# Kernel optimization log

Measured on AMD Instinct MI355X. Metric: run time of the kernel, lower is better.

The kernel has to match this reference:

```python
import jax, jax.numpy as jnp
import numpy as np

PAD = 32      # person_attrs_dim
NZ = 64       # num_zones
T = 32768     # number of timesteps
D = PAD + 1 + NZ  # 97, input dim to the MLP


def _ln(x, g, b, eps=1e-5):
    # LayerNorm over the last (only) axis of a 1-D vector
    m = jnp.mean(x)
    v = jnp.mean((x - m) ** 2)
    return g * (x - m) / jnp.sqrt(v + eps) + b


def setup_inputs() -> dict:
    key = jax.random.key(0)
    ks = jax.random.split(key, 24)

    def xav(k, shape):  # xavier_normal_ for nn.Linear weight [out, in]
        std = np.sqrt(2.0 / (shape[0] + shape[1])).astype(np.float32)
        return std * jax.random.normal(k, shape, dtype=jnp.float32)

    def lng(k, n):  # layernorm gain (perturbed from 1 so grads are non-trivial)
        return 1.0 + 0.1 * jax.random.normal(k, (n,), dtype=jnp.float32)

    def lnb(k, n):
        return 0.1 * jax.random.normal(k, (n,), dtype=jnp.float32)

    inp = {
        "person_attrs": jax.random.normal(ks[0], (PAD,), dtype=jnp.float32),
        "times": jax.random.uniform(ks[1], (T,), dtype=jnp.float32) * 24.0,
        "zone_features": jax.random.normal(ks[2], (NZ, 16), dtype=jnp.float32),
        "edge_index": jax.random.randint(ks[3], (2, 256), 0, NZ, dtype=jnp.int32),
        # input_norm
        "g0": lng(ks[4], D), "b0": lnb(ks[5], D),
        # encoder1: Linear(D,256) + LN(256)
        "W1": xav(ks[6], (256, D)), "b1": jnp.zeros((256,), jnp.float32),
        "g1": lng(ks[7], 256), "be1": lnb(ks[8], 256),
        # encoder2: Linear(256,128) + LN(128)
        "W2": xav(ks[9], (128, 256)), "b2": jnp.zeros((128,), jnp.float32),
        "g2": lng(ks[10], 128), "be2": lnb(ks[11], 128),
        # output_layer: Linear(128,64) + LN(64) + Linear(64,NZ)
        "W3": xav(ks[12], (64, 128)), "b3": jnp.zeros((64,), jnp.float32),
        "g3": lng(ks[13], 64), "be3": lnb(ks[14], 64),
        "W4": xav(ks[15], (NZ, 64)), "b4": jnp.zeros((NZ,), jnp.float32),
    }
    return inp


def reference(person_attrs, times, zone_features, edge_index,
              g0, b0, W1, b1, g1, be1, W2, b2, g2, be2,
              W3, b3, g3, be3, W4, b4):
    nz = W4.shape[0]
    # set_graph_data: symmetric adjacency with self-loops (zone_features unused)
    u, v = edge_index[0], edge_index[1]
    A = jnp.zeros((nz, nz), jnp.float32).at[u, v].set(1.0).at[v, u].set(1.0)
    A = jnp.maximum(A, jnp.eye(nz, dtype=jnp.float32))

    def step(zone, t):
        onehot = jax.nn.one_hot(zone, nz, dtype=jnp.float32)
        x = jnp.concatenate([person_attrs, t[None], onehot])  # [D]
        x = _ln(x, g0, b0)
        h = jax.nn.relu(_ln(W1 @ x + b1, g1, be1))   # dropout is eval-mode identity
        h = jax.nn.relu(_ln(W2 @ h + b2, g2, be2))
        h = jax.nn.relu(_ln(W3 @ h + b3, g3, be3))
        raw = W4 @ h + b4                            # [nz] raw logits
        row = A[zone]
        # (raw/temp with invalid=-50/temp) * temp  ==  where(valid, raw, -50)
        pred = jnp.where(row > 0, raw, jnp.float32(-50.0))
        nxt = jnp.argmax(jnp.where(row > 0, raw, -jnp.inf)).astype(zone.dtype)
        return nxt, pred

    _, zone_logits = jax.lax.scan(step, jnp.array(0, jnp.int32), times)
    return zone_logits  # [T, nz]
```

## Files before the change

kernel.cpp:

```cpp
#include <hip/hip_runtime.h>
#include <stdint.h>

typedef __attribute__((ext_vector_type(8))) short bf16x8;
typedef __attribute__((ext_vector_type(4))) float f32x4;
typedef __attribute__((ext_vector_type(4))) unsigned int u32x4;
typedef __attribute__((ext_vector_type(2))) unsigned int u32x2;

#define MFMA(a, b, c) __builtin_amdgcn_mfma_f32_16x16x32_bf16(a, b, c, 0, 0, 0)

__device__ __forceinline__ unsigned short f2b(float x) {
  unsigned u = __float_as_uint(x);
  return (unsigned short)((u + 0x7fffu + ((u >> 16) & 1u)) >> 16);
}
__device__ __forceinline__ float b2f(unsigned short h) {
  return __uint_as_float(((unsigned)h) << 16);
}

struct u2 { unsigned hi, lo; };
__device__ __forceinline__ u2 split2(float h0, float h1) {
  unsigned u0 = __float_as_uint(h0), u1 = __float_as_uint(h1);
  u2 r;
  r.hi = (u0 >> 16) | (u1 & 0xffff0000u);
  float r0 = h0 - __uint_as_float(u0 & 0xffff0000u);
  float r1 = h1 - __uint_as_float(u1 & 0xffff0000u);
  r.lo = (__float_as_uint(r0) >> 16) | (__float_as_uint(r1) & 0xffff0000u);
  return r;
}

#define SWZ(row, col) ((col) ^ ((((row) >> 2) & 1) << 4) ^ ((((row) >> 3) & 1) << 2))


__global__ void k_prep(const float* __restrict__ pa, const float* __restrict__ g0,
                       const float* __restrict__ b0, const float* __restrict__ W1,
                       const float* __restrict__ b1,
                       float* __restrict__ c_pa, float* __restrict__ w_t,
                       float* __restrict__ c_g, float* __restrict__ c_const,
                       float* __restrict__ scal, float* __restrict__ wzT,
                       float* __restrict__ wzZ) {
  int j = threadIdx.x;
  const float* wr = W1 + j * 97;
  float cg = 0.f, cc = 0.f, cp = 0.f;
  for (int k = 0; k < 97; ++k) { float w = wr[k]; cg += w * g0[k]; cc += w * b0[k]; }
  for (int k = 0; k < 32; ++k) cp += wr[k] * g0[k] * pa[k];
  c_g[j] = cg;
  c_const[j] = cc + b1[j];
  c_pa[j] = cp;
  w_t[j] = wr[32] * g0[32];
  for (int z = 0; z < 64; ++z) {
    float v = wr[33 + z] * g0[33 + z];
    wzT[j * 64 + z] = v;
    wzZ[z * 256 + j] = v;
  }
  if (j == 0) {
    float s = 0.f, q = 0.f;
    for (int k = 0; k < 32; ++k) { float x = pa[k]; s += x; q += x * x; }
    scal[0] = s; scal[1] = q;
  }
}

__global__ void k_prep2(const float* __restrict__ c_pa, const float* __restrict__ w_t,
                        const float* __restrict__ c_g, const float* __restrict__ c_const,
                        const float* __restrict__ wzT, float* __restrict__ st) {
  int tid = threadIdx.x;
  if (tid < 64) {
    int z = tid;
    float A = 0.f, Q = 0.f, dpa = 0.f, dwt = 0.f, dcg = 0.f, dcc = 0.f;
    for (int k = 0; k < 256; ++k) {
      float wz = wzT[k * 64 + z];
      A += wz; Q = fmaf(wz, wz, Q);
      dpa = fmaf(c_pa[k], wz, dpa);
      dwt = fmaf(w_t[k], wz, dwt);
      dcg = fmaf(c_g[k], wz, dcg);
      dcc = fmaf(c_const[k], wz, dcc);
    }
    st[z] = A; st[64 + z] = Q; st[128 + z] = dpa;
    st[192 + z] = dwt; st[256 + z] = dcg; st[320 + z] = dcc;
  } else {
    int lane = tid - 64;
    float acc[14];
    #pragma unroll
    for (int m = 0; m < 14; ++m) acc[m] = 0.f;
    for (int k = lane; k < 256; k += 64) {
      float P = c_pa[k], W = w_t[k], G = c_g[k], C = c_const[k];
      acc[0] += P; acc[1] += W; acc[2] += G; acc[3] += C;
      acc[4] = fmaf(P, P, acc[4]); acc[5] = fmaf(P, W, acc[5]);
      acc[6] = fmaf(P, G, acc[6]); acc[7] = fmaf(P, C, acc[7]);
      acc[8] = fmaf(W, W, acc[8]); acc[9] = fmaf(W, G, acc[9]);
      acc[10] = fmaf(W, C, acc[10]); acc[11] = fmaf(G, G, acc[11]);
      acc[12] = fmaf(G, C, acc[12]); acc[13] = fmaf(C, C, acc[13]);
    }
    #pragma unroll
    for (int off = 1; off < 64; off <<= 1) {
      #pragma unroll
      for (int m = 0; m < 14; ++m) acc[m] += __shfl_xor(acc[m], off, 64);
    }
    if (lane == 0) {
      #pragma unroll
      for (int m = 0; m < 14; ++m) st[386 + m] = acc[m];
    }
  }
}

__global__ void k_scal2st(const float* __restrict__ scal, float* __restrict__ st) {
  if (threadIdx.x < 2) st[384 + threadIdx.x] = scal[threadIdx.x];
}

__global__ void k_adj(const int* __restrict__ ei, unsigned long long* __restrict__ adj) {
  int t = threadIdx.x;
  if (t < 64) adj[t] = 1ull << t;
  __syncthreads();
  int u = ei[t] & 63, v = ei[256 + t] & 63;
  atomicOr(&adj[u], 1ull << v);
  atomicOr(&adj[v], 1ull << u);
}

__global__ void k_wsplit(const float* __restrict__ W2, const float* __restrict__ W3,
                         const float* __restrict__ W4,
                         unsigned short* __restrict__ W2Ah, unsigned short* __restrict__ W2Al,
                         unsigned short* __restrict__ W3Ah, unsigned short* __restrict__ W3Al,
                         unsigned short* __restrict__ W4Ah, unsigned short* __restrict__ W4Al) {
  int idx = blockIdx.x * 256 + threadIdx.x;
  float w; unsigned short* ph; unsigned short* pl; int o;
  if (idx < 32768) {
    int mt = idx >> 12, kt = (idx >> 9) & 7, lane = (idx >> 3) & 63, j = idx & 7;
    int m = mt * 16 + (lane & 15), k = kt * 32 + (lane >> 4) * 8 + j;
    w = W2[m * 256 + k]; ph = W2Ah; pl = W2Al; o = idx;
  } else if (idx < 40960) {
    int r = idx - 32768;
    int mt = r >> 11, kt = (r >> 9) & 3, lane = (r >> 3) & 63, j = r & 7;
    int m = mt * 16 + (lane & 15), k = kt * 32 + (lane >> 4) * 8 + j;
    w = W3[m * 128 + k]; ph = W3Ah; pl = W3Al; o = r;
  } else if (idx < 45056) {
    int r = idx - 40960;
    int mt = r >> 10, kt = (r >> 9) & 1, lane = (r >> 3) & 63, j = r & 7;
    int m = mt * 16 + (lane & 15), k = kt * 32 + (lane >> 4) * 8 + j;
    w = W4[m * 64 + k]; ph = W4Ah; pl = W4Al; o = r;
  } else return;
  unsigned short hb = f2b(w);
  ph[o] = hb;
  pl[o] = f2b(w - b2f(hb));
}


__global__ __launch_bounds__(256, 5) void k_pass1(
    const float* __restrict__ times,
    const float* __restrict__ c_pa, const float* __restrict__ w_t,
    const float* __restrict__ c_g, const float* __restrict__ c_const,
    const float* __restrict__ wzT, const float* __restrict__ st,
    const unsigned short* __restrict__ W2Ah, const unsigned short* __restrict__ W2Al,
    const unsigned short* __restrict__ W3Ah, const unsigned short* __restrict__ W3Al,
    const unsigned short* __restrict__ W4Ah, const unsigned short* __restrict__ W4Al,
    const float* __restrict__ b2, const float* __restrict__ b3,
    const float* __restrict__ b4,
    const float* __restrict__ g1, const float* __restrict__ be1,
    const float* __restrict__ g2, const float* __restrict__ be2,
    const float* __restrict__ g3, const float* __restrict__ be3,
    const unsigned long long* __restrict__ adj,
    unsigned char* __restrict__ nxt) {
  __shared__ __align__(16) char region[16384];
  __shared__ float u_lds[256];
  __shared__ float ps[512];

  unsigned short* Bhi = (unsigned short*)region;
  unsigned short* Blo = (unsigned short*)(region + 8192);
  unsigned long long* pk = (unsigned long long*)ps;

  const int tid = threadIdx.x;
  const int lane = tid & 63;
  const int l15 = lane & 15;
  const int lhi = lane >> 4;
  const int w = __builtin_amdgcn_readfirstlane(tid >> 6);
  const int i = blockIdx.x;

  const float t = times[i];
  const float m0 = (st[384] + t + 1.0f) * (1.0f / 97.0f);
  const float e2 = (st[385] + t * t + 1.0f) * (1.0f / 97.0f);
  const float alpha = 1.0f / sqrtf(e2 - m0 * m0 + 1e-5f);
  const float gma = -m0 * alpha;

  const f32x4 zero4 = {0.f, 0.f, 0.f, 0.f};

  {
    int k = tid;
    float u = fmaf(t, w_t[k], c_pa[k]);
    u = fmaf(alpha, u, c_const[k]);
    u = fmaf(gma, c_g[k], u);
    u_lds[k] = u;
    float su = u, sq = u * u;
    #pragma unroll
    for (int off = 1; off < 64; off <<= 1) {
      su += __shfl_xor(su, off, 64);
      sq += __shfl_xor(sq, off, 64);
    }
    if (lane == 0) { ps[w] = su; ps[256 + w] = sq; }
  }
  __syncthreads();
  float mu1, inv1;
  {
    float U1 = ps[0] + ps[1] + ps[2] + ps[3];
    float Qu = ps[256] + ps[257] + ps[258] + ps[259];
    float A1 = st[lane], Qz = st[64 + lane];
    float dpa = st[128 + lane], dwt = st[192 + lane];
    float dcg = st[256 + lane], dcc = st[320 + lane];
    float s1 = fmaf(alpha, A1, U1);
    float uwz = fmaf(alpha, fmaf(t, dwt, dpa), fmaf(gma, dcg, dcc));
    float s2 = Qu + 2.0f * alpha * uwz + alpha * alpha * Qz;
    mu1 = s1 * (1.0f / 256.0f);
    inv1 = 1.0f / sqrtf(s2 * (1.0f / 256.0f) - mu1 * mu1 + 1e-5f);
  }

  f32x4 acc[2][4];
  #pragma unroll
  for (int a = 0; a < 2; ++a)
    #pragma unroll
    for (int b = 0; b < 4; ++b) acc[a][b] = zero4;

  for (int kc = 0; kc < 4; ++kc) {
    if (kc) __syncthreads();
    #pragma unroll
    for (int q = 0; q < 2; ++q) {
      int o = w * 2 + q;
      int kb = kc * 64 + o * 8;
      f32x4 u0 = *(const f32x4*)(u_lds + kb);
      f32x4 u1v = *(const f32x4*)(u_lds + kb + 4);
      float hbuf[8];
      #pragma unroll
      for (int j = 0; j < 8; ++j) {
        int k = kb + j;
        float u = (j < 4) ? u0[j] : u1v[j - 4];
        float p = fmaf(alpha, wzT[k * 64 + lane], u);
        float gi = g1[k] * inv1;
        float bb = fmaf(-mu1, gi, be1[k]);
        hbuf[j] = fmaxf(fmaf(p, gi, bb), 0.f);
      }
      u32x4 vh, vl;
      #pragma unroll
      for (int e = 0; e < 4; ++e) {
        u2 s = split2(hbuf[2 * e], hbuf[2 * e + 1]);
        vh[e] = s.hi; vl[e] = s.lo;
      }
      int slotd = (((o >> 2) * 4 + lhi) * 64 + (o & 3) * 16 + l15) * 4;
      *(u32x4*)((unsigned*)Bhi + slotd) = vh;
      *(u32x4*)((unsigned*)Blo + slotd) = vl;
    }
    __syncthreads();
    #pragma unroll
    for (int kt = 0; kt < 2; ++kt) {
      int ktg = kc * 2 + kt;
      bf16x8 a0h = *(const bf16x8*)(W2Ah + (((2 * w + 0) * 8 + ktg) * 64 + lane) * 8);
      bf16x8 a0l = *(const bf16x8*)(W2Al + (((2 * w + 0) * 8 + ktg) * 64 + lane) * 8);
      bf16x8 a1h = *(const bf16x8*)(W2Ah + (((2 * w + 1) * 8 + ktg) * 64 + lane) * 8);
      bf16x8 a1l = *(const bf16x8*)(W2Al + (((2 * w + 1) * 8 + ktg) * 64 + lane) * 8);
      #pragma unroll
      for (int nt = 0; nt < 4; ++nt) {
        bf16x8 bh = *(const bf16x8*)(Bhi + ((kt * 4 + nt) * 64 + lane) * 8);
        bf16x8 bl = *(const bf16x8*)(Blo + ((kt * 4 + nt) * 64 + lane) * 8);
        acc[0][nt] = MFMA(a0h, bh, acc[0][nt]);
        acc[0][nt] = MFMA(a0h, bl, acc[0][nt]);
        acc[0][nt] = MFMA(a0l, bh, acc[0][nt]);
        acc[1][nt] = MFMA(a1h, bh, acc[1][nt]);
        acc[1][nt] = MFMA(a1h, bl, acc[1][nt]);
        acc[1][nt] = MFMA(a1l, bh, acc[1][nt]);
      }
    }
  }

  #pragma unroll
  for (int mti = 0; mti < 2; ++mti) {
    f32x4 bv = *(const f32x4*)(b2 + w * 32 + mti * 16 + lhi * 4);
    #pragma unroll
    for (int nt = 0; nt < 4; ++nt) acc[mti][nt] += bv;
  }
  #pragma unroll
  for (int nt = 0; nt < 4; ++nt) {
    float x1 = 0.f, x2 = 0.f;
    #pragma unroll
    for (int mti = 0; mti < 2; ++mti)
      #pragma unroll
      for (int r = 0; r < 4; ++r) { float v = acc[mti][nt][r]; x1 += v; x2 += v * v; }
    x1 += __shfl_xor(x1, 16, 64); x1 += __shfl_xor(x1, 32, 64);
    x2 += __shfl_xor(x2, 16, 64); x2 += __shfl_xor(x2, 32, 64);
    if (lane < 16) {
      ps[w * 64 + nt * 16 + lane] = x1;
      ps[256 + w * 64 + nt * 16 + lane] = x2;
    }
  }
  __syncthreads();
  if (w == 0) {
    int c = lane;
    float a = ps[c] + ps[64 + c] + ps[128 + c] + ps[192 + c];
    float b = ps[256 + c] + ps[320 + c] + ps[384 + c] + ps[448 + c];
    float mu = a * (1.0f / 128.0f);
    float inv = 1.0f / sqrtf(b * (1.0f / 128.0f) - mu * mu + 1e-5f);
    ps[c] = inv;
    ps[64 + c] = -mu * inv;
  }
  __syncthreads();

  f32x4 acc2[4];
  #pragma unroll
  for (int b = 0; b < 4; ++b) acc2[b] = zero4;

  for (int kc2 = 0; kc2 < 2; ++kc2) {
    if ((w >> 1) == kc2) {
      f32x4 g2v[2], be2v[2];
      #pragma unroll
      for (int mti = 0; mti < 2; ++mti) {
        g2v[mti]  = *(const f32x4*)(g2  + w * 32 + mti * 16 + lhi * 4);
        be2v[mti] = *(const f32x4*)(be2 + w * 32 + mti * 16 + lhi * 4);
      }
      #pragma unroll
      for (int nt = 0; nt < 4; ++nt) {
        int c = nt * 16 + l15;
        float P = ps[c], Q = ps[64 + c];
        #pragma unroll
        for (int mti = 0; mti < 2; ++mti) {
          float h[4];
          #pragma unroll
          for (int r = 0; r < 4; ++r) {
            float G = g2v[mti][r];
            h[r] = fmaxf(fmaf(acc[mti][nt][r], G * P, fmaf(G, Q, be2v[mti][r])), 0.f);
          }
          u2 s01 = split2(h[0], h[1]);
          u2 s23 = split2(h[2], h[3]);
          int base = (((w - 2 * kc2) * 4 + nt) * 64 +
                      (mti * 2 + (lhi >> 1)) * 16 + l15) * 8 + (lhi & 1) * 4;
          u32x2 vh = {s01.hi, s23.hi};
          u32x2 vl = {s01.lo, s23.lo};
          *(u32x2*)(Bhi + base) = vh;
          *(u32x2*)(Blo + base) = vl;
        }
      }
    }
    __syncthreads();
    #pragma unroll
    for (int kt = 0; kt < 2; ++kt) {
      int ktg = kc2 * 2 + kt;
      bf16x8 ah = *(const bf16x8*)(W3Ah + ((w * 4 + ktg) * 64 + lane) * 8);
      bf16x8 al = *(const bf16x8*)(W3Al + ((w * 4 + ktg) * 64 + lane) * 8);
      #pragma unroll
      for (int nt = 0; nt < 4; ++nt) {
        bf16x8 bh = *(const bf16x8*)(Bhi + ((kt * 4 + nt) * 64 + lane) * 8);
        bf16x8 bl = *(const bf16x8*)(Blo + ((kt * 4 + nt) * 64 + lane) * 8);
        acc2[nt] = MFMA(ah, bh, acc2[nt]);
        acc2[nt] = MFMA(ah, bl, acc2[nt]);
        acc2[nt] = MFMA(al, bh, acc2[nt]);
      }
    }
    __syncthreads();
  }

  {
    f32x4 bv = *(const f32x4*)(b3 + w * 16 + lhi * 4);
    #pragma unroll
    for (int nt = 0; nt < 4; ++nt) acc2[nt] += bv;
  }
  #pragma unroll
  for (int nt = 0; nt < 4; ++nt) {
    float x1 = 0.f, x2 = 0.f;
    #pragma unroll
    for (int r = 0; r < 4; ++r) { float v = acc2[nt][r]; x1 += v; x2 += v * v; }
    x1 += __shfl_xor(x1, 16, 64); x1 += __shfl_xor(x1, 32, 64);
    x2 += __shfl_xor(x2, 16, 64); x2 += __shfl_xor(x2, 32, 64);
    if (lane < 16) {
      ps[w * 64 + nt * 16 + lane] = x1;
      ps[256 + w * 64 + nt * 16 + lane] = x2;
    }
  }
  __syncthreads();
  if (w == 0) {
    int c = lane;
    float a = ps[c] + ps[64 + c] + ps[128 + c] + ps[192 + c];
    float b = ps[256 + c] + ps[320 + c] + ps[384 + c] + ps[448 + c];
    float mu = a * (1.0f / 64.0f);
    float inv = 1.0f / sqrtf(b * (1.0f / 64.0f) - mu * mu + 1e-5f);
    ps[c] = inv;
    ps[64 + c] = -mu * inv;
  }
  __syncthreads();

  {
    f32x4 g3v  = *(const f32x4*)(g3  + w * 16 + lhi * 4);
    f32x4 be3v = *(const f32x4*)(be3 + w * 16 + lhi * 4);
    #pragma unroll
    for (int nt = 0; nt < 4; ++nt) {
      int c = nt * 16 + l15;
      float P = ps[c], Q = ps[64 + c];
      float h[4];
      #pragma unroll
      for (int r = 0; r < 4; ++r) {
        float G = g3v[r];
        h[r] = fmaxf(fmaf(acc2[nt][r], G * P, fmaf(G, Q, be3v[r])), 0.f);
      }
      u2 s01 = split2(h[0], h[1]);
      u2 s23 = split2(h[2], h[3]);
      int base = (((w >> 1) * 4 + nt) * 64 +
                  ((w & 1) * 2 + (lhi >> 1)) * 16 + l15) * 8 + (lhi & 1) * 4;
      u32x2 vh = {s01.hi, s23.hi};
      u32x2 vl = {s01.lo, s23.lo};
      *(u32x2*)(Bhi + base) = vh;
      *(u32x2*)(Blo + base) = vl;
    }
  }
  __syncthreads();

  f32x4 acc3[4];
  #pragma unroll
  for (int b = 0; b < 4; ++b) acc3[b] = zero4;
  #pragma unroll
  for (int kt = 0; kt < 2; ++kt) {
    bf16x8 ah = *(const bf16x8*)(W4Ah + ((w * 2 + kt) * 64 + lane) * 8);
    bf16x8 al = *(const bf16x8*)(W4Al + ((w * 2 + kt) * 64 + lane) * 8);
    #pragma unroll
    for (int nt = 0; nt < 4; ++nt) {
      bf16x8 bh = *(const bf16x8*)(Bhi + ((kt * 4 + nt) * 64 + lane) * 8);
      bf16x8 bl = *(const bf16x8*)(Blo + ((kt * 4 + nt) * 64 + lane) * 8);
      acc3[nt] = MFMA(ah, bh, acc3[nt]);
      acc3[nt] = MFMA(ah, bl, acc3[nt]);
      acc3[nt] = MFMA(al, bh, acc3[nt]);
    }
  }
  f32x4 b4v = *(const f32x4*)(b4 + w * 16 + lhi * 4);
  unsigned long long kbest[4];
  #pragma unroll
  for (int nt = 0; nt < 4; ++nt) {
    unsigned long long am = adj[nt * 16 + l15];
    unsigned long long kb = 0ull;
    #pragma unroll
    for (int r = 0; r < 4; ++r) {
      int o = w * 16 + lhi * 4 + r;
      float raw = acc3[nt][r] + b4v[r];
      float val = ((am >> o) & 1ull) ? raw : -__builtin_huge_valf();
      unsigned u = __float_as_uint(val);
      u = (u & 0x80000000u) ? ~u : (u | 0x80000000u);
      unsigned long long key = ((unsigned long long)u << 6) | (unsigned long long)(63 - o);
      if (key > kb) kb = key;
    }
    unsigned long long oth = __shfl_xor(kb, 16, 64); if (oth > kb) kb = oth;
    oth = __shfl_xor(kb, 32, 64); if (oth > kb) kb = oth;
    kbest[nt] = kb;
  }
  if (lane < 16) {
    #pragma unroll
    for (int nt = 0; nt < 4; ++nt) pk[w * 64 + nt * 16 + lane] = kbest[nt];
  }
  __syncthreads();
  if (tid < 64) {
    unsigned long long k0 = pk[tid], k1 = pk[64 + tid];
    unsigned long long k2 = pk[128 + tid], k3 = pk[192 + tid];
    unsigned long long a = k0 > k1 ? k0 : k1;
    unsigned long long b = k2 > k3 ? k2 : k3;
    unsigned long long bb = a > b ? a : b;
    nxt[(size_t)i * 64 + tid] = (unsigned char)(63u - (unsigned)(bb & 63ull));
  }
}


__global__ void k_scan_a(const unsigned char* __restrict__ nxt,
                         unsigned char* __restrict__ cmap) {
  int c = blockIdx.x, lane = threadIdx.x;
  int g = lane;
  const unsigned char* p = nxt + (size_t)c * 128 * 64;
  for (int s = 0; s < 128; ++s) {
    int sig = p[s * 64 + lane];
    g = __shfl(sig, g, 64);
  }
  cmap[c * 64 + lane] = (unsigned char)g;
}

__global__ void k_scan_b(const unsigned char* __restrict__ cmap,
                         int* __restrict__ startz) {
  int lane = threadIdx.x;
  int cur = 0;
  for (int c = 0; c < 256; ++c) {
    if (lane == 0) startz[c] = cur;
    int row = cmap[c * 64 + lane];
    cur = __shfl(row, cur, 64);
  }
}

__global__ void k_scan_c(const unsigned char* __restrict__ nxt,
                         const int* __restrict__ startz,
                         unsigned char* __restrict__ zones) {
  int c = blockIdx.x, lane = threadIdx.x;
  int cur = startz[c];
  const unsigned char* p = nxt + (size_t)c * 128 * 64;
  for (int s = 0; s < 128; ++s) {
    if (lane == 0) zones[c * 128 + s] = (unsigned char)cur;
    int row = p[s * 64 + lane];
    cur = __shfl(row, cur, 64);
  }
}


__global__ __launch_bounds__(256, 2) void k_pass2m(
    const float* __restrict__ times, const unsigned char* __restrict__ zones,
    const float* __restrict__ c_pa, const float* __restrict__ w_t,
    const float* __restrict__ c_g, const float* __restrict__ c_const,
    const float* __restrict__ wzZ, const float* __restrict__ st,
    const unsigned short* __restrict__ W2Ah, const unsigned short* __restrict__ W2Al,
    const unsigned short* __restrict__ W3Ah, const unsigned short* __restrict__ W3Al,
    const unsigned short* __restrict__ W4Ah, const unsigned short* __restrict__ W4Al,
    const float* __restrict__ b2, const float* __restrict__ b3,
    const float* __restrict__ b4,
    const float* __restrict__ g1, const float* __restrict__ be1,
    const float* __restrict__ g2, const float* __restrict__ be2,
    const float* __restrict__ g3, const float* __restrict__ be3,
    const unsigned long long* __restrict__ adj,
    float* __restrict__ out) {
  __shared__ __align__(16) char region[32768];
  __shared__ float ps1[256], ps2[256];
  __shared__ unsigned long long am_lds[64];

  unsigned short* B1hi = (unsigned short*)region;
  unsigned short* B1lo = (unsigned short*)(region + 16384);
  float* h2p = (float*)region;
  unsigned short* B2hi = (unsigned short*)region;
  unsigned short* B2lo = (unsigned short*)(region + 16384);
  float* h3p = (float*)region;
  unsigned short* B3hi = (unsigned short*)(region + 16384);
  unsigned short* B3lo = (unsigned short*)(region + 24576);
  float* outT = (float*)region;

  const int tid = threadIdx.x;
  const int lane = tid & 63;
  const int l15 = lane & 15;
  const int lhi = lane >> 4;
  const int w = __builtin_amdgcn_readfirstlane(tid >> 6);
  const int i0 = blockIdx.x * 64;

  const float t = times[i0 + lane];
  const int z = zones[i0 + lane];
  const int zrow = z << 8;
  if (tid < 64) am_lds[tid] = adj[zones[i0 + tid]];

  const float m0 = (st[384] + t + 1.0f) * (1.0f / 97.0f);
  const float e2 = (st[385] + t * t + 1.0f) * (1.0f / 97.0f);
  const float a0 = 1.0f / sqrtf(e2 - m0 * m0 + 1e-5f);
  const float a1 = a0 * t;
  const float a2 = -m0 * a0;

  float mu1, inv1;
  {
    float SP = st[386], SW = st[387], SG = st[388], SC = st[389];
    float PP = st[390], PW = st[391], PG = st[392], PC = st[393];
    float WW = st[394], WG = st[395], WC = st[396];
    float GG = st[397], GC = st[398], CC = st[399];
    float U1 = a0 * SP + a1 * SW + a2 * SG + SC;
    float s1 = fmaf(a0, st[z], U1);
    float Qu = a0 * a0 * PP + a1 * a1 * WW + a2 * a2 * GG + CC
             + 2.0f * (a0 * a1 * PW + a0 * a2 * PG + a0 * PC
                       + a1 * a2 * WG + a1 * WC + a2 * GC);
    float uwz = a0 * st[128 + z] + a1 * st[192 + z] + a2 * st[256 + z] + st[320 + z];
    float s2 = Qu + 2.0f * a0 * uwz + a0 * a0 * st[64 + z];
    mu1 = s1 * (1.0f / 256.0f);
    inv1 = 1.0f / sqrtf(s2 * (1.0f / 256.0f) - mu1 * mu1 + 1e-5f);
  }

  const f32x4 zero4 = {0.f, 0.f, 0.f, 0.f};
  f32x4 acc[2][4];
  #pragma unroll
  for (int a = 0; a < 2; ++a)
    #pragma unroll
    for (int b = 0; b < 4; ++b) acc[a][b] = zero4;

  for (int kc = 0; kc < 2; ++kc) {
    if (kc) __syncthreads();
    #pragma unroll
    for (int q = 0; q < 4; ++q) {
      int kb = kc * 128 + w * 32 + q * 8;
      float hbuf[8];
      #pragma unroll
      for (int j = 0; j < 8; ++j) {
        int k = kb + j;
        float u = fmaf(a0, c_pa[k], fmaf(a1, w_t[k], fmaf(a2, c_g[k], c_const[k])));
        float p = fmaf(a0, wzZ[zrow + k], u);
        float gi = g1[k] * inv1;
        float bb = fmaf(-mu1, gi, be1[k]);
        hbuf[j] = fmaxf(fmaf(p, gi, bb), 0.f);
      }
      u32x4 vh, vl;
      #pragma unroll
      for (int e = 0; e < 4; ++e) {
        u2 s = split2(hbuf[2 * e], hbuf[2 * e + 1]);
        vh[e] = s.hi; vl[e] = s.lo;
      }
      int slotd = ((w * 4 + lhi) * 64 + q * 16 + l15) * 4;
      *(u32x4*)((unsigned*)B1hi + slotd) = vh;
      *(u32x4*)((unsigned*)B1lo + slotd) = vl;
    }
    __syncthreads();
    for (int kt = 0; kt < 4; ++kt) {
      int ktg = kc * 4 + kt;
      bf16x8 a0h = *(const bf16x8*)(W2Ah + (((2 * w + 0) * 8 + ktg) * 64 + lane) * 8);
      bf16x8 a0l = *(const bf16x8*)(W2Al + (((2 * w + 0) * 8 + ktg) * 64 + lane) * 8);
      bf16x8 a1h = *(const bf16x8*)(W2Ah + (((2 * w + 1) * 8 + ktg) * 64 + lane) * 8);
      bf16x8 a1l = *(const bf16x8*)(W2Al + (((2 * w + 1) * 8 + ktg) * 64 + lane) * 8);
      #pragma unroll
      for (int nt = 0; nt < 4; ++nt) {
        bf16x8 bh = *(const bf16x8*)(B1hi + ((kt * 4 + nt) * 64 + lane) * 8);
        bf16x8 bl = *(const bf16x8*)(B1lo + ((kt * 4 + nt) * 64 + lane) * 8);
        acc[0][nt] = MFMA(a0h, bh, acc[0][nt]);
        acc[0][nt] = MFMA(a0h, bl, acc[0][nt]);
        acc[0][nt] = MFMA(a0l, bh, acc[0][nt]);
        acc[1][nt] = MFMA(a1h, bh, acc[1][nt]);
        acc[1][nt] = MFMA(a1h, bl, acc[1][nt]);
        acc[1][nt] = MFMA(a1l, bh, acc[1][nt]);
      }
    }
  }
  #pragma unroll
  for (int mti = 0; mti < 2; ++mti) {
    f32x4 bv = *(const f32x4*)(b2 + w * 32 + mti * 16 + lhi * 4);
    #pragma unroll
    for (int nt = 0; nt < 4; ++nt) acc[mti][nt] += bv;
  }
  {
    float sa[4], sb[4];
    #pragma unroll
    for (int nt = 0; nt < 4; ++nt) {
      float x1 = 0.f, x2 = 0.f;
      #pragma unroll
      for (int mti = 0; mti < 2; ++mti)
        #pragma unroll
        for (int r = 0; r < 4; ++r) { float v = acc[mti][nt][r]; x1 += v; x2 += v * v; }
      x1 += __shfl_xor(x1, 16, 64); x1 += __shfl_xor(x1, 32, 64);
      x2 += __shfl_xor(x2, 16, 64); x2 += __shfl_xor(x2, 32, 64);
      sa[nt] = x1; sb[nt] = x2;
    }
    if (lane < 16) {
      #pragma unroll
      for (int nt = 0; nt < 4; ++nt) {
        ps1[w * 64 + nt * 16 + lane] = sa[nt];
        ps2[w * 64 + nt * 16 + lane] = sb[nt];
      }
    }
  }
  __syncthreads();
  #pragma unroll
  for (int mti = 0; mti < 2; ++mti)
    #pragma unroll
    for (int nt = 0; nt < 4; ++nt)
      #pragma unroll
      for (int r = 0; r < 4; ++r) {
        int row = w * 32 + mti * 16 + lhi * 4 + r;
        h2p[row * 64 + SWZ(row, nt * 16 + l15)] = acc[mti][nt][r];
      }
  __syncthreads();

  float mu2, inv2;
  {
    float a = ps1[lane] + ps1[64 + lane] + ps1[128 + lane] + ps1[192 + lane];
    float b = ps2[lane] + ps2[64 + lane] + ps2[128 + lane] + ps2[192 + lane];
    mu2 = a * (1.0f / 128.0f);
    inv2 = 1.0f / sqrtf(b * (1.0f / 128.0f) - mu2 * mu2 + 1e-5f);
  }
  float hv[32];
  #pragma unroll
  for (int mi = 0; mi < 32; ++mi) {
    int row = w * 32 + mi;
    hv[mi] = h2p[row * 64 + SWZ(row, lane)];
  }
  __syncthreads();
  #pragma unroll
  for (int q = 0; q < 4; ++q) {
    float hbuf[8];
    #pragma unroll
    for (int j = 0; j < 8; ++j) {
      int mi = q * 8 + j, mm = w * 32 + mi;
      float gi = g2[mm] * inv2;
      float bb = fmaf(-mu2, gi, be2[mm]);
      hbuf[j] = fmaxf(fmaf(hv[mi], gi, bb), 0.f);
    }
    u32x4 vh, vl;
    #pragma unroll
    for (int e = 0; e < 4; ++e) {
      u2 s = split2(hbuf[2 * e], hbuf[2 * e + 1]);
      vh[e] = s.hi; vl[e] = s.lo;
    }
    int slotd = ((w * 4 + lhi) * 64 + q * 16 + l15) * 4;
    *(u32x4*)((unsigned*)B2hi + slotd) = vh;
    *(u32x4*)((unsigned*)B2lo + slotd) = vl;
  }
  __syncthreads();

  f32x4 acc2[4];
  #pragma unroll
  for (int b = 0; b < 4; ++b) acc2[b] = zero4;
  for (int kt = 0; kt < 4; ++kt) {
    bf16x8 ah = *(const bf16x8*)(W3Ah + ((w * 4 + kt) * 64 + lane) * 8);
    bf16x8 al = *(const bf16x8*)(W3Al + ((w * 4 + kt) * 64 + lane) * 8);
    #pragma unroll
    for (int nt = 0; nt < 4; ++nt) {
      bf16x8 bh = *(const bf16x8*)(B2hi + ((kt * 4 + nt) * 64 + lane) * 8);
      bf16x8 bl = *(const bf16x8*)(B2lo + ((kt * 4 + nt) * 64 + lane) * 8);
      acc2[nt] = MFMA(ah, bh, acc2[nt]);
      acc2[nt] = MFMA(ah, bl, acc2[nt]);
      acc2[nt] = MFMA(al, bh, acc2[nt]);
    }
  }
  {
    f32x4 bv = *(const f32x4*)(b3 + w * 16 + lhi * 4);
    #pragma unroll
    for (int nt = 0; nt < 4; ++nt) acc2[nt] += bv;
  }
  {
    float sa[4], sb[4];
    #pragma unroll
    for (int nt = 0; nt < 4; ++nt) {
      float x1 = 0.f, x2 = 0.f;
      #pragma unroll
      for (int r = 0; r < 4; ++r) { float v = acc2[nt][r]; x1 += v; x2 += v * v; }
      x1 += __shfl_xor(x1, 16, 64); x1 += __shfl_xor(x1, 32, 64);
      x2 += __shfl_xor(x2, 16, 64); x2 += __shfl_xor(x2, 32, 64);
      sa[nt] = x1; sb[nt] = x2;
    }
    if (lane < 16) {
      #pragma unroll
      for (int nt = 0; nt < 4; ++nt) {
        ps1[w * 64 + nt * 16 + lane] = sa[nt];
        ps2[w * 64 + nt * 16 + lane] = sb[nt];
      }
    }
  }
  __syncthreads();
  #pragma unroll
  for (int nt = 0; nt < 4; ++nt)
    #pragma unroll
    for (int r = 0; r < 4; ++r) {
      int row = w * 16 + lhi * 4 + r;
      h3p[row * 64 + SWZ(row, nt * 16 + l15)] = acc2[nt][r];
    }
  __syncthreads();

  float mu3, inv3;
  {
    float a = ps1[lane] + ps1[64 + lane] + ps1[128 + lane] + ps1[192 + lane];
    float b = ps2[lane] + ps2[64 + lane] + ps2[128 + lane] + ps2[192 + lane];
    mu3 = a * (1.0f / 64.0f);
    inv3 = 1.0f / sqrtf(b * (1.0f / 64.0f) - mu3 * mu3 + 1e-5f);
  }
  #pragma unroll
  for (int q = 0; q < 2; ++q) {
    int o = w * 2 + q;
    float hbuf[8];
    #pragma unroll
    for (int j = 0; j < 8; ++j) {
      int mm = o * 8 + j;
      float v = h3p[mm * 64 + SWZ(mm, lane)];
      float gi = g3[mm] * inv3;
      float bb = fmaf(-mu3, gi, be3[mm]);
      hbuf[j] = fmaxf(fmaf(v, gi, bb), 0.f);
    }
    u32x4 vh, vl;
    #pragma unroll
    for (int e = 0; e < 4; ++e) {
      u2 s = split2(hbuf[2 * e], hbuf[2 * e + 1]);
      vh[e] = s.hi; vl[e] = s.lo;
    }
    int slotd = (((o >> 2) * 4 + lhi) * 64 + (o & 3) * 16 + l15) * 4;
    *(u32x4*)((unsigned*)B3hi + slotd) = vh;
    *(u32x4*)((unsigned*)B3lo + slotd) = vl;
  }
  __syncthreads();

  f32x4 acc3[4];
  #pragma unroll
  for (int b = 0; b < 4; ++b) acc3[b] = zero4;
  for (int kt = 0; kt < 2; ++kt) {
    bf16x8 ah = *(const bf16x8*)(W4Ah + ((w * 2 + kt) * 64 + lane) * 8);
    bf16x8 al = *(const bf16x8*)(W4Al + ((w * 2 + kt) * 64 + lane) * 8);
    #pragma unroll
    for (int nt = 0; nt < 4; ++nt) {
      bf16x8 bh = *(const bf16x8*)(B3hi + ((kt * 4 + nt) * 64 + lane) * 8);
      bf16x8 bl = *(const bf16x8*)(B3lo + ((kt * 4 + nt) * 64 + lane) * 8);
      acc3[nt] = MFMA(ah, bh, acc3[nt]);
      acc3[nt] = MFMA(ah, bl, acc3[nt]);
      acc3[nt] = MFMA(al, bh, acc3[nt]);
    }
  }
  f32x4 b4v = *(const f32x4*)(b4 + w * 16 + lhi * 4);
  #pragma unroll
  for (int nt = 0; nt < 4; ++nt) {
    unsigned long long am = am_lds[nt * 16 + l15];
    #pragma unroll
    for (int r = 0; r < 4; ++r) {
      int o = w * 16 + lhi * 4 + r;
      float raw = acc3[nt][r] + b4v[r];
      float predv = ((am >> o) & 1ull) ? raw : -50.0f;
      int b = nt * 16 + l15;
      outT[b * 64 + SWZ(b, o)] = predv;
    }
  }
  __syncthreads();
  {
    int b = tid >> 2, cb = (tid & 3) * 16;
    size_t gbase = ((size_t)(i0 + b)) * 64 + cb;
    #pragma unroll
    for (int c4 = 0; c4 < 4; ++c4) {
      int col = cb + c4 * 4;
      f32x4 v = *(const f32x4*)(outT + b * 64 + SWZ(b, col));
      *(f32x4*)(out + gbase + c4 * 4) = v;
    }
  }
}


extern "C" void kernel_launch(void* const* d_in, const int* in_sizes, int n_in,
                              void* d_out, int out_size, void* d_ws, size_t ws_size,
                              hipStream_t stream) {
  const float* pa    = (const float*)d_in[0];
  const float* times = (const float*)d_in[1];
  const int*   ei    = (const int*)d_in[3];
  const float* g0    = (const float*)d_in[4];
  const float* b0    = (const float*)d_in[5];
  const float* W1    = (const float*)d_in[6];
  const float* b1    = (const float*)d_in[7];
  const float* g1    = (const float*)d_in[8];
  const float* be1   = (const float*)d_in[9];
  const float* W2    = (const float*)d_in[10];
  const float* b2    = (const float*)d_in[11];
  const float* g2    = (const float*)d_in[12];
  const float* be2   = (const float*)d_in[13];
  const float* W3    = (const float*)d_in[14];
  const float* b3    = (const float*)d_in[15];
  const float* g3    = (const float*)d_in[16];
  const float* be3   = (const float*)d_in[17];
  const float* W4    = (const float*)d_in[18];
  const float* b4    = (const float*)d_in[19];

  char* ws = (char*)d_ws;
  float* c_pa    = (float*)(ws + 0);
  float* w_t     = (float*)(ws + 1024);
  float* c_g     = (float*)(ws + 2048);
  float* c_const = (float*)(ws + 3072);
  float* scal    = (float*)(ws + 4096);
  unsigned long long* adj = (unsigned long long*)(ws + 4608);
  float* wzT = (float*)(ws + 5120);
  float* wzZ = (float*)(ws + 70656);
  unsigned short* W2Ah = (unsigned short*)(ws + 136192);
  unsigned short* W2Al = (unsigned short*)(ws + 201728);
  unsigned short* W3Ah = (unsigned short*)(ws + 267264);
  unsigned short* W3Al = (unsigned short*)(ws + 283648);
  unsigned short* W4Ah = (unsigned short*)(ws + 300032);
  unsigned short* W4Al = (unsigned short*)(ws + 308224);
  float* st = (float*)(ws + 316416);
  unsigned char* nxt  = (unsigned char*)(ws + 318464);
  unsigned char* cmap = (unsigned char*)(ws + 2415616);
  int* startz = (int*)(ws + 2432000);
  unsigned char* zones = (unsigned char*)(ws + 2433024);

  k_prep<<<1, 256, 0, stream>>>(pa, g0, b0, W1, b1, c_pa, w_t, c_g, c_const,
                                scal, wzT, wzZ);
  k_prep2<<<1, 128, 0, stream>>>(c_pa, w_t, c_g, c_const, wzT, st);
  k_scal2st<<<1, 64, 0, stream>>>(scal, st);
  k_adj<<<1, 256, 0, stream>>>(ei, adj);
  k_wsplit<<<176, 256, 0, stream>>>(W2, W3, W4, W2Ah, W2Al, W3Ah, W3Al, W4Ah, W4Al);
  k_pass1<<<32768, 256, 0, stream>>>(times, c_pa, w_t, c_g, c_const, wzT, st,
                                     W2Ah, W2Al, W3Ah, W3Al, W4Ah, W4Al,
                                     b2, b3, b4, g1, be1, g2, be2, g3, be3,
                                     adj, nxt);
  k_scan_a<<<256, 64, 0, stream>>>(nxt, cmap);
  k_scan_b<<<1, 64, 0, stream>>>(cmap, startz);
  k_scan_c<<<256, 64, 0, stream>>>(nxt, startz, zones);
  k_pass2m<<<512, 256, 0, stream>>>(times, zones, c_pa, w_t, c_g, c_const,
                                    wzZ, st, W2Ah, W2Al, W3Ah, W3Al, W4Ah, W4Al,
                                    b2, b3, b4, g1, be1, g2, be2, g3, be3,
                                    adj, (float*)d_out);
}
```

Baseline: 793.4 us.

## Merge setup kernels, use v_perm for bf16 split, refactor layer-1 LN math

Fuses four tiny single-block setup kernels (prep, prep2, scal2st, adj) into one k_setup kernel with __syncthreads between phases, removing three launches and their serialization gaps. The bf16 hi/lo packing in split2 now uses a single byte-permute builtin instead of shift/mask/or sequences. In pass1, the layer-1 LayerNorm inner loop is restructured to precompute alpha*g1 and g1*u into LDS, reducing per-element multiplies. This costs an extra LDS array and relies on the intra-block sync being correct for wzT reads written by other threads in the same kernel, since those writes go through global memory.

```diff
diff --git a/kernel.cpp b/kernel.cpp
--- a/kernel.cpp
+++ b/kernel.cpp
@@ -20,50 +20,47 @@
 __device__ __forceinline__ u2 split2(float h0, float h1) {
   unsigned u0 = __float_as_uint(h0), u1 = __float_as_uint(h1);
   u2 r;
-  r.hi = (u0 >> 16) | (u1 & 0xffff0000u);
+  r.hi = __builtin_amdgcn_perm(u1, u0, 0x07060302u);
   float r0 = h0 - __uint_as_float(u0 & 0xffff0000u);
   float r1 = h1 - __uint_as_float(u1 & 0xffff0000u);
-  r.lo = (__float_as_uint(r0) >> 16) | (__float_as_uint(r1) & 0xffff0000u);
+  r.lo = __builtin_amdgcn_perm(__float_as_uint(r1), __float_as_uint(r0), 0x07060302u);
   return r;
 }
 
 #define SWZ(row, col) ((col) ^ ((((row) >> 2) & 1) << 4) ^ ((((row) >> 3) & 1) << 2))
 
 
-__global__ void k_prep(const float* __restrict__ pa, const float* __restrict__ g0,
-                       const float* __restrict__ b0, const float* __restrict__ W1,
-                       const float* __restrict__ b1,
-                       float* __restrict__ c_pa, float* __restrict__ w_t,
-                       float* __restrict__ c_g, float* __restrict__ c_const,
-                       float* __restrict__ scal, float* __restrict__ wzT,
-                       float* __restrict__ wzZ) {
+__global__ void k_setup(const float* __restrict__ pa, const float* __restrict__ g0,
+                        const float* __restrict__ b0, const float* __restrict__ W1,
+                        const float* __restrict__ b1, const int* __restrict__ ei,
+                        float* __restrict__ c_pa, float* __restrict__ w_t,
+                        float* __restrict__ c_g, float* __restrict__ c_const,
+                        float* __restrict__ wzT, float* __restrict__ wzZ,
+                        float* __restrict__ st, unsigned long long* __restrict__ adj) {
   int j = threadIdx.x;
-  const float* wr = W1 + j * 97;
-  float cg = 0.f, cc = 0.f, cp = 0.f;
-  for (int k = 0; k < 97; ++k) { float w = wr[k]; cg += w * g0[k]; cc += w * b0[k]; }
-  for (int k = 0; k < 32; ++k) cp += wr[k] * g0[k] * pa[k];
-  c_g[j] = cg;
-  c_const[j] = cc + b1[j];
-  c_pa[j] = cp;
-  w_t[j] = wr[32] * g0[32];
-  for (int z = 0; z < 64; ++z) {
-    float v = wr[33 + z] * g0[33 + z];
-    wzT[j * 64 + z] = v;
-    wzZ[z * 256 + j] = v;
-  }
-  if (j == 0) {
-    float s = 0.f, q = 0.f;
-    for (int k = 0; k < 32; ++k) { float x = pa[k]; s += x; q += x * x; }
-    scal[0] = s; scal[1] = q;
-  }
-}
-
-__global__ void k_prep2(const float* __restrict__ c_pa, const float* __restrict__ w_t,
-                        const float* __restrict__ c_g, const float* __restrict__ c_const,
-                        const float* __restrict__ wzT, float* __restrict__ st) {
-  int tid = threadIdx.x;
-  if (tid < 64) {
-    int z = tid;
+  {
+    const float* wr = W1 + j * 97;
+    float cg = 0.f, cc = 0.f, cp = 0.f;
+    for (int k = 0; k < 97; ++k) { float w = wr[k]; cg += w * g0[k]; cc += w * b0[k]; }
+    for (int k = 0; k < 32; ++k) cp += wr[k] * g0[k] * pa[k];
+    c_g[j] = cg;
+    c_const[j] = cc + b1[j];
+    c_pa[j] = cp;
+    w_t[j] = wr[32] * g0[32];
+    for (int z = 0; z < 64; ++z) {
+      float v = wr[33 + z] * g0[33 + z];
+      wzT[j * 64 + z] = v;
+      wzZ[z * 256 + j] = v;
+    }
+    if (j == 0) {
+      float s = 0.f, q = 0.f;
+      for (int k = 0; k < 32; ++k) { float x = pa[k]; s += x; q += x * x; }
+      st[384] = s; st[385] = q;
+    }
+  }
+  __syncthreads();
+  if (j < 64) {
+    int z = j;
     float A = 0.f, Q = 0.f, dpa = 0.f, dwt = 0.f, dcg = 0.f, dcc = 0.f;
     for (int k = 0; k < 256; ++k) {
       float wz = wzT[k * 64 + z];
@@ -75,8 +72,8 @@
     }
     st[z] = A; st[64 + z] = Q; st[128 + z] = dpa;
     st[192 + z] = dwt; st[256 + z] = dcg; st[320 + z] = dcc;
-  } else {
-    int lane = tid - 64;
+  } else if (j < 128) {
+    int lane = j - 64;
     float acc[14];
     #pragma unroll
     for (int m = 0; m < 14; ++m) acc[m] = 0.f;
@@ -99,17 +96,9 @@
       for (int m = 0; m < 14; ++m) st[386 + m] = acc[m];
     }
   }
-}
-
-__global__ void k_scal2st(const float* __restrict__ scal, float* __restrict__ st) {
-  if (threadIdx.x < 2) st[384 + threadIdx.x] = scal[threadIdx.x];
-}
-
-__global__ void k_adj(const int* __restrict__ ei, unsigned long long* __restrict__ adj) {
-  int t = threadIdx.x;
-  if (t < 64) adj[t] = 1ull << t;
-  __syncthreads();
-  int u = ei[t] & 63, v = ei[256 + t] & 63;
+  if (j < 64) adj[j] = 1ull << j;
+  __syncthreads();
+  int u = ei[j] & 63, v = ei[256 + j] & 63;
   atomicOr(&adj[u], 1ull << v);
   atomicOr(&adj[v], 1ull << u);
 }
@@ -158,7 +147,8 @@
     const unsigned long long* __restrict__ adj,
     unsigned char* __restrict__ nxt) {
   __shared__ __align__(16) char region[16384];
-  __shared__ float u_lds[256];
+  __shared__ float G_lds[256];
+  __shared__ float W_lds[256];
   __shared__ float ps[512];
 
   unsigned short* Bhi = (unsigned short*)region;
@@ -182,10 +172,12 @@
 
   {
     int k = tid;
+    float g1k = g1[k];
     float u = fmaf(t, w_t[k], c_pa[k]);
     u = fmaf(alpha, u, c_const[k]);
     u = fmaf(gma, c_g[k], u);
-    u_lds[k] = u;
+    G_lds[k] = alpha * g1k;
+    W_lds[k] = g1k * u;
     float su = u, sq = u * u;
     #pragma unroll
     for (int off = 1; off < 64; off <<= 1) {
@@ -221,17 +213,19 @@
     for (int q = 0; q < 2; ++q) {
       int o = w * 2 + q;
       int kb = kc * 64 + o * 8;
-      f32x4 u0 = *(const f32x4*)(u_lds + kb);
-      f32x4 u1v = *(const f32x4*)(u_lds + kb + 4);
+      f32x4 G0 = *(const f32x4*)(G_lds + kb);
+      f32x4 G1 = *(const f32x4*)(G_lds + kb + 4);
+      f32x4 W0 = *(const f32x4*)(W_lds + kb);
+      f32x4 W1v = *(const f32x4*)(W_lds + kb + 4);
       float hbuf[8];
       #pragma unroll
       for (int j = 0; j < 8; ++j) {
         int k = kb + j;
-        float u = (j < 4) ? u0[j] : u1v[j - 4];
-        float p = fmaf(alpha, wzT[k * 64 + lane], u);
-        float gi = g1[k] * inv1;
-        float bb = fmaf(-mu1, gi, be1[k]);
-        hbuf[j] = fmaxf(fmaf(p, gi, bb), 0.f);
+        float Gk = (j < 4) ? G0[j] : G1[j - 4];
+        float Wk = (j < 4) ? W0[j] : W1v[j - 4];
+        float t1 = fmaf(Gk, wzT[k * 64 + lane], Wk);
+        float t2 = fmaf(-g1[k], mu1, t1);
+        hbuf[j] = fmaxf(fmaf(inv1, t2, be1[k]), 0.f);
       }
       u32x4 vh, vl;
       #pragma unroll
@@ -834,7 +828,6 @@
   float* w_t     = (float*)(ws + 1024);
   float* c_g     = (float*)(ws + 2048);
   float* c_const = (float*)(ws + 3072);
-  float* scal    = (float*)(ws + 4096);
   unsigned long long* adj = (unsigned long long*)(ws + 4608);
   float* wzT = (float*)(ws + 5120);
   float* wzZ = (float*)(ws + 70656);
@@ -850,11 +843,8 @@
   int* startz = (int*)(ws + 2432000);
   unsigned char* zones = (unsigned char*)(ws + 2433024);
 
-  k_prep<<<1, 256, 0, stream>>>(pa, g0, b0, W1, b1, c_pa, w_t, c_g, c_const,
-                                scal, wzT, wzZ);
-  k_prep2<<<1, 128, 0, stream>>>(c_pa, w_t, c_g, c_const, wzT, st);
-  k_scal2st<<<1, 64, 0, stream>>>(scal, st);
-  k_adj<<<1, 256, 0, stream>>>(ei, adj);
+  k_setup<<<1, 256, 0, stream>>>(pa, g0, b0, W1, b1, ei, c_pa, w_t, c_g, c_const,
+                                 wzT, wzZ, st, adj);
   k_wsplit<<<176, 256, 0, stream>>>(W2, W3, W4, W2Ah, W2Al, W3Ah, W3Al, W4Ah, W4Al);
   k_pass1<<<32768, 256, 0, stream>>>(times, c_pa, w_t, c_g, c_const, wzT, st,
                                      W2Ah, W2Al, W3Ah, W3Al, W4Ah, W4Al,
```

Measured after the change: 784.1 us. No clear change (-1.2%).
